# Performance work log

Measured on AMD Instinct MI355X. Metric: run time of the kernel, lower is better.

## Reference

```python
import jax, jax.numpy as jnp
import numpy as np

N = 100000   # nodes
E = 1600000  # directed edges (before self loops)
IN = 64
HID = 32     # per-head hidden channels
H = 4        # heads
OUT = 32     # final output channels
NEG_SLOPE = 0.2
LN_EPS = 1e-5


def setup_inputs() -> dict:
    key = jax.random.key(0)
    ks = jax.random.split(key, 24)
    def nrm(k, shape, s=0.1):
        return jax.random.normal(k, shape, jnp.float32) * s
    inp = {
        "x": jax.random.normal(ks[0], (N, IN), jnp.float32),
        "edge_index": jax.random.randint(ks[1], (2, E), 0, N, jnp.int32),
    }
    in_dims = [IN, H * HID, H * HID]
    j = 2
    for i, di in enumerate(in_dims):
        inp[f"W{i}"] = nrm(ks[j], (di, H * HID)); j += 1
        inp[f"as{i}"] = nrm(ks[j], (H, HID)); j += 1
        inp[f"ad{i}"] = nrm(ks[j], (H, HID)); j += 1
        inp[f"b{i}"] = jnp.zeros((H * HID,), jnp.float32)
        inp[f"g{i}"] = jnp.ones((H * HID,), jnp.float32)
        inp[f"be{i}"] = jnp.zeros((H * HID,), jnp.float32)
    inp["Wf"] = nrm(ks[j], (H * HID, OUT)); j += 1
    inp["asf"] = nrm(ks[j], (1, OUT)); j += 1
    inp["adf"] = nrm(ks[j], (1, OUT)); j += 1
    inp["bf"] = jnp.zeros((OUT,), jnp.float32)
    return inp


def gat_conv(x, src, dst, W, att_s, att_d, bias, heads, C, concat, n_nodes):
    # h: [N, H, C]
    h = (x @ W).reshape(n_nodes, heads, C)
    a_src = jnp.sum(h * att_s, axis=-1)  # [N, H]
    a_dst = jnp.sum(h * att_d, axis=-1)  # [N, H]
    e = jax.nn.leaky_relu(a_src[src] + a_dst[dst], NEG_SLOPE)  # [E', H]
    # segment softmax over incoming edges of each dst node
    m = jax.ops.segment_max(e, dst, num_segments=n_nodes)
    m = jnp.where(jnp.isfinite(m), m, 0.0)
    ex = jnp.exp(e - m[dst])
    denom = jax.ops.segment_sum(ex, dst, num_segments=n_nodes)
    alpha = ex / (denom[dst] + 1e-16)  # [E', H]
    msg = h[src] * alpha[..., None]    # [E', H, C]
    out = jax.ops.segment_sum(msg, dst, num_segments=n_nodes)  # [N, H, C]
    if concat:
        out = out.reshape(n_nodes, heads * C)
    else:
        out = out.mean(axis=1)
    return out + bias


def layer_norm(x, g, b):
    mu = x.mean(-1, keepdims=True)
    v = jnp.mean((x - mu) ** 2, axis=-1, keepdims=True)
    return g * (x - mu) / jnp.sqrt(v + LN_EPS) + b


def reference(x, edge_index,
              W0, as0, ad0, b0, g0, be0,
              W1, as1, ad1, b1, g1, be1,
              W2, as2, ad2, b2, g2, be2,
              Wf, asf, adf, bf):
    n_nodes = x.shape[0]
    loop = jnp.arange(n_nodes, dtype=edge_index.dtype)
    src = jnp.concatenate([edge_index[0], loop])  # add self loops (PyG default)
    dst = jnp.concatenate([edge_index[1], loop])
    blocks = [(W0, as0, ad0, b0, g0, be0),
              (W1, as1, ad1, b1, g1, be1),
              (W2, as2, ad2, b2, g2, be2)]
    for (W, a_s, a_d, b, g, be) in blocks:
        x = gat_conv(x, src, dst, W, a_s, a_d, b, H, HID, True, n_nodes)
        x = jax.nn.elu(layer_norm(x, g, be))
    return gat_conv(x, src, dst, Wf, asf, adf, bf, 1, OUT, False, n_nodes)
```

## Files before the change

### kernel.cpp

```cpp
#include <hip/hip_runtime.h>
#include <hip/hip_fp16.h>

constexpr int NN   = 100000;
constexpr int EE   = 1600000;
constexpr int ETOT = EE + NN;
constexpr float SLOPE = 0.2f;
constexpr int BSH = 10;
constexpr int NB  = (NN + (1 << BSH) - 1) >> BSH;
constexpr int CCH = 8192;
constexpr int DCAP  = 36;
constexpr int DCAPP = 37;

typedef __attribute__((ext_vector_type(8))) short short8;
typedef __attribute__((ext_vector_type(4))) float f32x4;

__device__ __forceinline__ unsigned short f2h(float f) {
    __half h = __float2half(f);
    return *(unsigned short*)&h;
}
__device__ __forceinline__ float h_lo(unsigned u) {
    unsigned short s = u & 0xffff;
    return __half2float(*(__half*)&s);
}
__device__ __forceinline__ float h_hi(unsigned u) {
    unsigned short s = u >> 16;
    return __half2float(*(__half*)&s);
}
__device__ __forceinline__ void wave_lds_fence() {
    __asm__ volatile("s_waitcnt lgkmcnt(0)" ::: "memory");
}
__device__ __forceinline__ void pk8(__half2* acc2, uint4 u, __half2 a2) {
    acc2[0] = __hfma2(*(__half2*)&u.x, a2, acc2[0]);
    acc2[1] = __hfma2(*(__half2*)&u.y, a2, acc2[1]);
    acc2[2] = __hfma2(*(__half2*)&u.z, a2, acc2[2]);
    acc2[3] = __hfma2(*(__half2*)&u.w, a2, acc2[3]);
}
__device__ __forceinline__ void fma8f(float* acc, uint4 u, float al) {
    acc[0] += h_lo(u.x) * al; acc[1] += h_hi(u.x) * al;
    acc[2] += h_lo(u.y) * al; acc[3] += h_hi(u.y) * al;
    acc[4] += h_lo(u.z) * al; acc[5] += h_hi(u.z) * al;
    acc[6] += h_lo(u.w) * al; acc[7] += h_hi(u.w) * al;
}

__global__ void k_cvt_x(const float* __restrict__ x, unsigned short* __restrict__ xb) {
    int i = blockIdx.x * blockDim.x + threadIdx.x;
    if (i >= NN * 64 / 8) return;
    const float4* xp = (const float4*)(x + (size_t)i * 8);
    float4 v0 = xp[0], v1 = xp[1];
    unsigned short o[8] = {f2h(v0.x), f2h(v0.y), f2h(v0.z), f2h(v0.w),
                           f2h(v1.x), f2h(v1.y), f2h(v1.z), f2h(v1.w)};
    *(uint4*)(xb + (size_t)i * 8) = *(uint4*)o;
}

__global__ void k_cvt_wt(const float* __restrict__ W, unsigned short* __restrict__ Wt,
                         int K, int N) {
    int i = blockIdx.x * blockDim.x + threadIdx.x;
    if (i >= K * N) return;
    int k = i / N, n = i % N;
    Wt[(size_t)n * K + k] = f2h(W[i]);
}

__global__ void k_zero(int* p, int n) {
    int i = blockIdx.x * blockDim.x + threadIdx.x;
    if (i < n) p[i] = 0;
}

__global__ __launch_bounds__(256) void k_bhist(const int* __restrict__ ei,
                                               int* __restrict__ gbh) {
    __shared__ int h[NB];
    int t = threadIdx.x;
    if (t < NB) h[t] = 0;
    __syncthreads();
    int i = blockIdx.x * 2048 + t;
#pragma unroll
    for (int k = 0; k < 8; k++, i += 256)
        if (i < EE) atomicAdd(&h[ei[EE + i] >> BSH], 1);
    __syncthreads();
    if (t < NB && h[t]) atomicAdd(&gbh[t], h[t]);
}

__global__ void k_bscan(const int* __restrict__ gbh, int* __restrict__ ebase,
                        int* __restrict__ gcur) {
    __shared__ int sd[128];
    int t = threadIdx.x;
    int v = (t < NB) ? gbh[t] : 0;
    sd[t] = v;
    __syncthreads();
    for (int off = 1; off < 128; off <<= 1) {
        int x = (t >= off) ? sd[t - off] : 0;
        __syncthreads();
        sd[t] += x;
        __syncthreads();
    }
    int ex = sd[t] - v;
    if (t < NB) { ebase[t] = ex; gcur[t] = ex; }
    if (t == NB) ebase[NB] = EE;
}

__global__ __launch_bounds__(256) void k_bscatter(const int* __restrict__ ei,
                                                  int* __restrict__ gcur,
                                                  int* __restrict__ pbuf) {
    __shared__ int h[NB], base[NB], cur[NB];
    int t = threadIdx.x;
    if (t < NB) { h[t] = 0; cur[t] = 0; }
    __syncthreads();
    int c0 = blockIdx.x * CCH;
    int cend = c0 + CCH < EE ? c0 + CCH : EE;
    for (int i = c0 + t; i < cend; i += 256)
        atomicAdd(&h[ei[EE + i] >> BSH], 1);
    __syncthreads();
    if (t < NB && h[t] > 0) base[t] = atomicAdd(&gcur[t], h[t]);
    __syncthreads();
    for (int i = c0 + t; i < cend; i += 256) {
        int s = ei[i], d = ei[EE + i];
        int b = d >> BSH;
        int c = atomicAdd(&cur[b], 1);
        pbuf[base[b] + c] = s | ((d & ((1 << BSH) - 1)) << 17);
    }
}

__global__ __launch_bounds__(256) void k_bcsr(const int* __restrict__ pbuf,
                                              const int* __restrict__ ebase,
                                              int* __restrict__ row_ptr,
                                              int* __restrict__ esrc) {
    constexpr int BNODES = 1 << BSH;
    __shared__ int hist[BNODES];
    __shared__ int cur[BNODES];
    __shared__ int sd[256];
    int b = blockIdx.x, t = threadIdx.x;
    int node0 = b << BSH;
    int e0 = ebase[b], e1 = ebase[b + 1];
    for (int i = t; i < BNODES; i += 256) { hist[i] = 0; cur[i] = 0; }
    __syncthreads();
    for (int i = e0 + t; i < e1; i += 256)
        atomicAdd(&hist[pbuf[i] >> 17], 1);
    __syncthreads();
    int s0 = hist[4 * t], s1 = hist[4 * t + 1], s2 = hist[4 * t + 2], s3 = hist[4 * t + 3];
    int ts = s0 + s1 + s2 + s3;
    sd[t] = ts;
    __syncthreads();
    for (int off = 1; off < 256; off <<= 1) {
        int x = (t >= off) ? sd[t - off] : 0;
        __syncthreads();
        sd[t] += x;
        __syncthreads();
    }
    int ex = sd[t] - ts;
    hist[4 * t] = ex;
    hist[4 * t + 1] = ex + s0;
    hist[4 * t + 2] = ex + s0 + s1;
    hist[4 * t + 3] = ex + s0 + s1 + s2;
    __syncthreads();
    int rbase = e0 + node0;
    for (int nl = t; nl < BNODES; nl += 256) {
        int n = node0 + nl;
        if (n < NN) {
            int rp = rbase + hist[nl] + nl;
            row_ptr[n] = rp;
            esrc[rp] = n;
        }
    }
    __syncthreads();
    for (int i = e0 + t; i < e1; i += 256) {
        int p = pbuf[i];
        int nl = p >> 17;
        int c = atomicAdd(&cur[nl], 1);
        esrc[rbase + hist[nl] + nl + 1 + c] = p & 0x1FFFF;
    }
}

template <int BN, int H>
__global__ __launch_bounds__(256) void k_mfma_att(
    const unsigned short* __restrict__ Ab, const unsigned short* __restrict__ Bt,
    const float* __restrict__ as_, const float* __restrict__ ad_,
    unsigned short* __restrict__ hb, float* __restrict__ a_s,
    float* __restrict__ a_d, int M, int K) {
    constexpr int NCT = BN / 16;
    constexpr int LDK = 72;
    __shared__ unsigned short As[128 * LDK];
    __shared__ unsigned short Bs[BN * LDK];
    int tid = threadIdx.x;
    int lane = tid & 63, w = tid >> 6;
    int q = lane >> 4, col = lane & 15;
    int rowBase = blockIdx.x * 128;

    f32x4 acc[2][NCT];
#pragma unroll
    for (int rt = 0; rt < 2; rt++)
#pragma unroll
        for (int ct = 0; ct < NCT; ct++) acc[rt][ct] = (f32x4){0.f, 0.f, 0.f, 0.f};

    int u = tid & 7;
    int r0 = tid >> 3;
    int nph = K >> 6;
    for (int ph = 0; ph < nph; ph++) {
        int kof = ph * 64 + u * 8;
#pragma unroll
        for (int rr = r0; rr < 128; rr += 32) {
            int gr = rowBase + rr;
            uint4 v = make_uint4(0, 0, 0, 0);
            if (gr < M) v = *(const uint4*)(Ab + (size_t)gr * K + kof);
            *(uint4*)(&As[rr * LDK + u * 8]) = v;
        }
#pragma unroll
        for (int br = r0; br < BN; br += 32) {
            uint4 v = *(const uint4*)(Bt + (size_t)br * K + kof);
            *(uint4*)(&Bs[br * LDK + u * 8]) = v;
        }
        __syncthreads();

        short8 af[2][2];
#pragma unroll
        for (int rt = 0; rt < 2; rt++)
#pragma unroll
            for (int kt = 0; kt < 2; kt++)
                af[rt][kt] = *(const short8*)(&As[(w * 32 + rt * 16 + col) * LDK + kt * 32 + q * 8]);
#pragma unroll
        for (int kt = 0; kt < 2; kt++)
#pragma unroll
            for (int ct = 0; ct < NCT; ct++) {
                short8 bf = *(const short8*)(&Bs[(ct * 16 + col) * LDK + kt * 32 + q * 8]);
#pragma unroll
                for (int rt = 0; rt < 2; rt++)
                    acc[rt][ct] = __builtin_amdgcn_mfma_f32_16x16x32_f16(
                        af[rt][kt], bf, acc[rt][ct], 0, 0, 0);
            }
        __syncthreads();
    }

    float swv[NCT], dwv[NCT];
#pragma unroll
    for (int ct = 0; ct < NCT; ct++) {
        int c = ct * 16 + col;
        swv[ct] = as_[c];
        dwv[ct] = ad_[c];
    }
#pragma unroll
    for (int rt = 0; rt < 2; rt++) {
#pragma unroll
        for (int r = 0; r < 4; r++) {
            int gr = rowBase + w * 32 + rt * 16 + q * 4 + r;
            if constexpr (H == 4) {
                float ps[4] = {0, 0, 0, 0}, pd[4] = {0, 0, 0, 0};
#pragma unroll
                for (int ct = 0; ct < NCT; ct++) {
                    float v = acc[rt][ct][r];
                    ps[ct >> 1] += v * swv[ct];
                    pd[ct >> 1] += v * dwv[ct];
                }
#pragma unroll
                for (int m = 1; m < 16; m <<= 1)
#pragma unroll
                    for (int h = 0; h < 4; h++) {
                        ps[h] += __shfl_xor(ps[h], m);
                        pd[h] += __shfl_xor(pd[h], m);
                    }
                if (gr < M) {
#pragma unroll
                    for (int ct = 0; ct < NCT; ct++)
                        hb[(size_t)gr * BN + ct * 16 + col] = f2h(acc[rt][ct][r]);
                    if (col == 0) {
                        *(float4*)(a_s + (size_t)gr * 4) = make_float4(ps[0], ps[1], ps[2], ps[3]);
                        *(float4*)(a_d + (size_t)gr * 4) = make_float4(pd[0], pd[1], pd[2], pd[3]);
                    }
                }
            } else {
                float ps = 0.f, pd = 0.f;
#pragma unroll
                for (int ct = 0; ct < NCT; ct++) {
                    float v = acc[rt][ct][r];
                    ps += v * swv[ct];
                    pd += v * dwv[ct];
                }
#pragma unroll
                for (int m = 1; m < 16; m <<= 1) {
                    ps += __shfl_xor(ps, m);
                    pd += __shfl_xor(pd, m);
                }
                if (gr < M) {
#pragma unroll
                    for (int ct = 0; ct < NCT; ct++)
                        hb[(size_t)gr * BN + ct * 16 + col] = f2h(acc[rt][ct][r]);
                    if (col == 0) { a_s[gr] = ps; a_d[gr] = pd; }
                }
            }
        }
    }
}

__global__ __launch_bounds__(256) void k_aggregate_ln(
    const unsigned short* __restrict__ hb, const float* __restrict__ a_src,
    const float* __restrict__ a_dst, const int* __restrict__ row_ptr,
    const int* __restrict__ esrc, const float* __restrict__ bias,
    const float* __restrict__ gamma, const float* __restrict__ beta,
    unsigned short* __restrict__ xb) {
    __shared__ uint2 slab_all[4][4 * 4 * DCAPP];
    int tid = threadIdx.x;
    int w = tid >> 6, lane = tid & 63;
    int g = lane >> 4, i = lane & 15;
    int myhead = i >> 2;
    uint2* slab = slab_all[w];
    int n0 = blockIdx.x * 16 + w * 4;
    int n = n0 + g;
    bool valid = n < NN;
    int start = 0, deg = 0;
    if (valid) {
        start = row_ptr[n];
        int end = (n == NN - 1) ? ETOT : row_ptr[n + 1];
        deg = end - start;
    }
    int wmax = deg;
#pragma unroll
    for (int m = 1; m < 64; m <<= 1) wmax = max(wmax, __shfl_xor(wmax, m));

    if (wmax <= DCAP) {
        float4 ad = make_float4(0.f, 0.f, 0.f, 0.f);
        if (valid) ad = ((const float4*)a_dst)[n];
        float d0 = 0.f, d1 = 0.f, d2 = 0.f, d3 = 0.f;
        uint2* nslab = slab + g * (4 * DCAPP);
        for (int k = i; k < deg; k += 16) {
            int s = esrc[start + k];
            float4 a = ((const float4*)a_src)[s];
            float e0 = a.x + ad.x; e0 = fmaxf(e0, SLOPE * e0); float x0 = __expf(e0);
            float e1 = a.y + ad.y; e1 = fmaxf(e1, SLOPE * e1); float x1 = __expf(e1);
            float e2 = a.z + ad.z; e2 = fmaxf(e2, SLOPE * e2); float x2 = __expf(e2);
            float e3 = a.w + ad.w; e3 = fmaxf(e3, SLOPE * e3); float x3 = __expf(e3);
            nslab[0 * DCAPP + k] = make_uint2((unsigned)s, __float_as_uint(x0));
            nslab[1 * DCAPP + k] = make_uint2((unsigned)s, __float_as_uint(x1));
            nslab[2 * DCAPP + k] = make_uint2((unsigned)s, __float_as_uint(x2));
            nslab[3 * DCAPP + k] = make_uint2((unsigned)s, __float_as_uint(x3));
            d0 += x0; d1 += x1; d2 += x2; d3 += x3;
        }
#pragma unroll
        for (int m = 1; m < 16; m <<= 1) {
            d0 += __shfl_xor(d0, m);
            d1 += __shfl_xor(d1, m);
            d2 += __shfl_xor(d2, m);
            d3 += __shfl_xor(d3, m);
        }
        float dh = myhead == 0 ? d0 : myhead == 1 ? d1 : myhead == 2 ? d2 : d3;
        float inv = 1.f / (dh + 1e-16f);
        wave_lds_fence();

        __half2 acc2[4];
#pragma unroll
        for (int k = 0; k < 4; k++) acc2[k] = __float2half2_rn(0.f);
        const uint2* myrow = nslab + myhead * DCAPP;
        const unsigned short* hbase = hb + i * 8;
        int j = 0;
        for (; j + 4 <= deg; j += 4) {
            uint2 p0 = myrow[j], p1 = myrow[j + 1], p2 = myrow[j + 2], p3 = myrow[j + 3];
            uint4 u0 = *(const uint4*)(hbase + (size_t)p0.x * 128);
            uint4 u1 = *(const uint4*)(hbase + (size_t)p1.x * 128);
            uint4 u2 = *(const uint4*)(hbase + (size_t)p2.x * 128);
            uint4 u3 = *(const uint4*)(hbase + (size_t)p3.x * 128);
            pk8(acc2, u0, __float2half2_rn(__uint_as_float(p0.y)));
            pk8(acc2, u1, __float2half2_rn(__uint_as_float(p1.y)));
            pk8(acc2, u2, __float2half2_rn(__uint_as_float(p2.y)));
            pk8(acc2, u3, __float2half2_rn(__uint_as_float(p3.y)));
        }
        for (; j < deg; j++) {
            uint2 p = myrow[j];
            uint4 uu = *(const uint4*)(hbase + (size_t)p.x * 128);
            pk8(acc2, uu, __float2half2_rn(__uint_as_float(p.y)));
        }
        float acc[8];
#pragma unroll
        for (int k = 0; k < 4; k++) {
            float2 f = __half22float2(acc2[k]);
            acc[2 * k] = f.x * inv;
            acc[2 * k + 1] = f.y * inv;
        }

        if (valid) {
            float y[8];
            float sum = 0.f;
            const float4* bp = (const float4*)(bias + i * 8);
            float4 b0 = bp[0], b1 = bp[1];
#pragma unroll
            for (int k = 0; k < 8; k++) {
                float b = k < 4 ? (&b0.x)[k] : (&b1.x)[k - 4];
                y[k] = acc[k] + b;
                sum += y[k];
            }
#pragma unroll
            for (int m = 1; m < 16; m <<= 1) sum += __shfl_xor(sum, m);
            float mu = sum * (1.f / 128.f);
            float ss = 0.f;
            float d[8];
#pragma unroll
            for (int k = 0; k < 8; k++) { d[k] = y[k] - mu; ss += d[k] * d[k]; }
#pragma unroll
            for (int m = 1; m < 16; m <<= 1) ss += __shfl_xor(ss, m);
            float is = rsqrtf(ss * (1.f / 128.f) + 1e-5f);
            const float4* gp = (const float4*)(gamma + i * 8);
            const float4* ep = (const float4*)(beta + i * 8);
            float4 g0 = gp[0], g1 = gp[1], e0 = ep[0], e1 = ep[1];
            unsigned short o16[8];
#pragma unroll
            for (int k = 0; k < 8; k++) {
                float gm = k < 4 ? (&g0.x)[k] : (&g1.x)[k - 4];
                float bt = k < 4 ? (&e0.x)[k] : (&e1.x)[k - 4];
                float z = gm * (d[k] * is) + bt;
                o16[k] = f2h(z > 0.f ? z : __expf(z) - 1.f);
            }
            *(uint4*)(xb + (size_t)n * 128 + i * 8) = *(uint4*)o16;
        }
    } else {
        for (int m4 = 0; m4 < 4; m4++) {
            int nm = n0 + m4;
            if (nm >= NN) continue;
            int startm = row_ptr[nm];
            int endm = (nm == NN - 1) ? ETOT : row_ptr[nm + 1];
            int degm = endm - startm;
            float4 ad = ((const float4*)a_dst)[nm];
            int gg = lane >> 4, c16 = lane & 15, hh = c16 >> 2;
            float acc[8];
#pragma unroll
            for (int k = 0; k < 8; k++) acc[k] = 0.f;
            if (degm <= 64) {
                int msrc = 0;
                float me0 = 0.f, me1 = 0.f, me2 = 0.f, me3 = 0.f;
                if (lane < degm) {
                    int s = esrc[startm + lane];
                    msrc = s;
                    float4 a = ((const float4*)a_src)[s];
                    float e0 = a.x + ad.x; e0 = fmaxf(e0, SLOPE * e0); me0 = __expf(e0);
                    float e1 = a.y + ad.y; e1 = fmaxf(e1, SLOPE * e1); me1 = __expf(e1);
                    float e2 = a.z + ad.z; e2 = fmaxf(e2, SLOPE * e2); me2 = __expf(e2);
                    float e3 = a.w + ad.w; e3 = fmaxf(e3, SLOPE * e3); me3 = __expf(e3);
                }
                float d0 = me0, d1 = me1, d2 = me2, d3 = me3;
#pragma unroll
                for (int m = 1; m < 64; m <<= 1) {
                    d0 += __shfl_xor(d0, m);
                    d1 += __shfl_xor(d1, m);
                    d2 += __shfl_xor(d2, m);
                    d3 += __shfl_xor(d3, m);
                }
                me0 *= 1.f / (d0 + 1e-16f);
                me1 *= 1.f / (d1 + 1e-16f);
                me2 *= 1.f / (d2 + 1e-16f);
                me3 *= 1.f / (d3 + 1e-16f);
                int iters = (degm + 3) >> 2;
                for (int it = 0; it < iters; it++) {
                    int j = gg + (it << 2);
                    int jj = j < degm ? j : 0;
                    int s = __shfl(msrc, jj);
                    float a0 = __shfl(me0, jj), a1 = __shfl(me1, jj);
                    float a2 = __shfl(me2, jj), a3 = __shfl(me3, jj);
                    if (j < degm) {
                        float al = hh == 0 ? a0 : hh == 1 ? a1 : hh == 2 ? a2 : a3;
                        uint4 uu = *(const uint4*)(hb + (size_t)s * 128 + c16 * 8);
                        fma8f(acc, uu, al);
                    }
                }
            } else {
                float d0 = 0.f, d1 = 0.f, d2 = 0.f, d3 = 0.f;
                for (int k = startm + lane; k < endm; k += 64) {
                    int s = esrc[k];
                    float4 a = ((const float4*)a_src)[s];
                    float e0 = a.x + ad.x; e0 = fmaxf(e0, SLOPE * e0); d0 += __expf(e0);
                    float e1 = a.y + ad.y; e1 = fmaxf(e1, SLOPE * e1); d1 += __expf(e1);
                    float e2 = a.z + ad.z; e2 = fmaxf(e2, SLOPE * e2); d2 += __expf(e2);
                    float e3 = a.w + ad.w; e3 = fmaxf(e3, SLOPE * e3); d3 += __expf(e3);
                }
#pragma unroll
                for (int m = 1; m < 64; m <<= 1) {
                    d0 += __shfl_xor(d0, m);
                    d1 += __shfl_xor(d1, m);
                    d2 += __shfl_xor(d2, m);
                    d3 += __shfl_xor(d3, m);
                }
                float invh = hh == 0 ? 1.f / (d0 + 1e-16f) : hh == 1 ? 1.f / (d1 + 1e-16f)
                           : hh == 2 ? 1.f / (d2 + 1e-16f) : 1.f / (d3 + 1e-16f);
                float adh = hh == 0 ? ad.x : hh == 1 ? ad.y : hh == 2 ? ad.z : ad.w;
                for (int j = gg; j < degm; j += 4) {
                    int s = esrc[startm + j];
                    float e = a_src[(size_t)s * 4 + hh] + adh;
                    e = fmaxf(e, SLOPE * e);
                    float al = __expf(e) * invh;
                    uint4 uu = *(const uint4*)(hb + (size_t)s * 128 + c16 * 8);
                    fma8f(acc, uu, al);
                }
            }
#pragma unroll
            for (int k = 0; k < 8; k++) {
                acc[k] += __shfl_xor(acc[k], 16);
                acc[k] += __shfl_xor(acc[k], 32);
            }
            if (lane < 16) {
                float y[8];
                float sum = 0.f;
                const float4* bp = (const float4*)(bias + lane * 8);
                float4 b0 = bp[0], b1 = bp[1];
#pragma unroll
                for (int k = 0; k < 8; k++) {
                    float b = k < 4 ? (&b0.x)[k] : (&b1.x)[k - 4];
                    y[k] = acc[k] + b;
                    sum += y[k];
                }
#pragma unroll
                for (int m = 1; m < 16; m <<= 1) sum += __shfl_xor(sum, m);
                float mu = sum * (1.f / 128.f);
                float ss = 0.f;
                float d[8];
#pragma unroll
                for (int k = 0; k < 8; k++) { d[k] = y[k] - mu; ss += d[k] * d[k]; }
#pragma unroll
                for (int m = 1; m < 16; m <<= 1) ss += __shfl_xor(ss, m);
                float is = rsqrtf(ss * (1.f / 128.f) + 1e-5f);
                const float4* gp = (const float4*)(gamma + lane * 8);
                const float4* ep = (const float4*)(beta + lane * 8);
                float4 g0 = gp[0], g1 = gp[1], e0 = ep[0], e1 = ep[1];
                unsigned short o16[8];
#pragma unroll
                for (int k = 0; k < 8; k++) {
                    float gm = k < 4 ? (&g0.x)[k] : (&g1.x)[k - 4];
                    float bt = k < 4 ? (&e0.x)[k] : (&e1.x)[k - 4];
                    float z = gm * (d[k] * is) + bt;
                    o16[k] = f2h(z > 0.f ? z : __expf(z) - 1.f);
                }
                *(uint4*)(xb + (size_t)nm * 128 + lane * 8) = *(uint4*)o16;
            }
        }
    }
}

__global__ __launch_bounds__(256) void k_agg_final(
    const unsigned short* __restrict__ hb, const float* __restrict__ a_src,
    const float* __restrict__ a_dst, const int* __restrict__ row_ptr,
    const int* __restrict__ esrc, const float* __restrict__ bf,
    float* __restrict__ out) {
    __shared__ uint2 slab_all[4][64];
    int lane = threadIdx.x & 63;
    int w = threadIdx.x >> 6;
    uint2* slab = slab_all[w];
    int n = blockIdx.x * 4 + w;
    if (n >= NN) return;
    int start = row_ptr[n];
    int end = (n == NN - 1) ? ETOT : row_ptr[n + 1];
    int deg = end - start;
    float adn = a_dst[n];

    int g = lane >> 3, c8 = lane & 7;
    float acc[4] = {0.f, 0.f, 0.f, 0.f};

    if (deg <= 64) {
        int msrc = 0;
        float me = 0.f;
        if (lane < deg) {
            int s = esrc[start + lane];
            msrc = s;
            float e = a_src[s] + adn;
            e = fmaxf(e, SLOPE * e);
            me = __expf(e);
        }
        float d = me;
#pragma unroll
        for (int m = 1; m < 64; m <<= 1) d += __shfl_xor(d, m);
        float inv = 1.f / (d + 1e-16f);
        if (lane < deg) slab[lane] = make_uint2((unsigned)msrc, __float_as_uint(me));
        wave_lds_fence();
        __half2 acc2[2] = {__float2half2_rn(0.f), __float2half2_rn(0.f)};
        const unsigned short* hbase = hb + c8 * 4;
        int j = g;
        for (; j + 8 < deg; j += 16) {
            uint2 p0 = slab[j], p1 = slab[j + 8];
            uint2 u0 = *(const uint2*)(hbase + (size_t)p0.x * 32);
            uint2 u1 = *(const uint2*)(hbase + (size_t)p1.x * 32);
            __half2 a0 = __float2half2_rn(__uint_as_float(p0.y));
            __half2 a1 = __float2half2_rn(__uint_as_float(p1.y));
            acc2[0] = __hfma2(*(__half2*)&u0.x, a0, acc2[0]);
            acc2[1] = __hfma2(*(__half2*)&u0.y, a0, acc2[1]);
            acc2[0] = __hfma2(*(__half2*)&u1.x, a1, acc2[0]);
            acc2[1] = __hfma2(*(__half2*)&u1.y, a1, acc2[1]);
        }
        if (j < deg) {
            uint2 p = slab[j];
            uint2 u = *(const uint2*)(hbase + (size_t)p.x * 32);
            __half2 a2 = __float2half2_rn(__uint_as_float(p.y));
            acc2[0] = __hfma2(*(__half2*)&u.x, a2, acc2[0]);
            acc2[1] = __hfma2(*(__half2*)&u.y, a2, acc2[1]);
        }
        float2 f0 = __half22float2(acc2[0]);
        float2 f1 = __half22float2(acc2[1]);
        acc[0] = f0.x * inv; acc[1] = f0.y * inv;
        acc[2] = f1.x * inv; acc[3] = f1.y * inv;
    } else {
        float d = 0.f;
        for (int k = start + lane; k < end; k += 64) {
            int s = esrc[k];
            float e = a_src[s] + adn;
            e = fmaxf(e, SLOPE * e);
            d += __expf(e);
        }
#pragma unroll
        for (int m = 1; m < 64; m <<= 1) d += __shfl_xor(d, m);
        float inv = 1.f / (d + 1e-16f);
        for (int j = g; j < deg; j += 8) {
            int s = esrc[start + j];
            float e = a_src[s] + adn;
            e = fmaxf(e, SLOPE * e);
            float al = __expf(e) * inv;
            uint2 u = *(const uint2*)(hb + (size_t)s * 32 + c8 * 4);
            acc[0] += h_lo(u.x) * al; acc[1] += h_hi(u.x) * al;
            acc[2] += h_lo(u.y) * al; acc[3] += h_hi(u.y) * al;
        }
    }
#pragma unroll
    for (int k = 0; k < 4; k++) {
        acc[k] += __shfl_xor(acc[k], 8);
        acc[k] += __shfl_xor(acc[k], 16);
        acc[k] += __shfl_xor(acc[k], 32);
    }
    if (lane < 8) {
        float4 b4 = ((const float4*)bf)[lane];
        float4 o = make_float4(acc[0] + b4.x, acc[1] + b4.y, acc[2] + b4.z,
                               acc[3] + b4.w);
        ((float4*)out)[(size_t)n * 8 + lane] = o;
    }
}

extern "C" void kernel_launch(void* const* d_in, const int* in_sizes, int n_in,
                              void* d_out, int out_size, void* d_ws,
                              size_t ws_size, hipStream_t stream) {
    const float* x  = (const float*)d_in[0];
    const int* ei   = (const int*)d_in[1];
    const float* W[3]  = {(const float*)d_in[2], (const float*)d_in[8],  (const float*)d_in[14]};
    const float* AS[3] = {(const float*)d_in[3], (const float*)d_in[9],  (const float*)d_in[15]};
    const float* AD[3] = {(const float*)d_in[4], (const float*)d_in[10], (const float*)d_in[16]};
    const float* Bb[3] = {(const float*)d_in[5], (const float*)d_in[11], (const float*)d_in[17]};
    const float* G[3]  = {(const float*)d_in[6], (const float*)d_in[12], (const float*)d_in[18]};
    const float* BE[3] = {(const float*)d_in[7], (const float*)d_in[13], (const float*)d_in[19]};
    const float* Wf  = (const float*)d_in[20];
    const float* asf = (const float*)d_in[21];
    const float* adf = (const float*)d_in[22];
    const float* bfp = (const float*)d_in[23];
    float* out = (float*)d_out;

    unsigned short* xb = (unsigned short*)d_ws;
    unsigned short* hb = xb + (size_t)NN * 128;
    float* a_s = (float*)(hb + (size_t)NN * 128);
    float* a_d = a_s + (size_t)NN * 4;
    int* row_ptr = (int*)(a_d + (size_t)NN * 4);
    int* esrc    = row_ptr + NN;
    int* gbh     = esrc + ETOT;
    int* ebase   = gbh + NB;
    int* gcur    = ebase + NB + 1;
    int* pbuf    = gcur + NB;
    unsigned short* Wt0 = (unsigned short*)(pbuf + EE);
    unsigned short* Wt1 = Wt0 + 128 * 64;
    unsigned short* Wt2 = Wt1 + 128 * 128;
    unsigned short* Wtf = Wt2 + 128 * 128;

    k_cvt_x<<<(NN * 64 / 8 + 255) / 256, 256, 0, stream>>>(x, xb);
    k_cvt_wt<<<(64 * 128 + 255) / 256, 256, 0, stream>>>(W[0], Wt0, 64, 128);
    k_cvt_wt<<<(128 * 128 + 255) / 256, 256, 0, stream>>>(W[1], Wt1, 128, 128);
    k_cvt_wt<<<(128 * 128 + 255) / 256, 256, 0, stream>>>(W[2], Wt2, 128, 128);
    k_cvt_wt<<<(128 * 32 + 255) / 256, 256, 0, stream>>>(Wf, Wtf, 128, 32);

    k_zero<<<1, 128, 0, stream>>>(gbh, NB);
    k_bhist<<<(EE + 2047) / 2048, 256, 0, stream>>>(ei, gbh);
    k_bscan<<<1, 128, 0, stream>>>(gbh, ebase, gcur);
    k_bscatter<<<(EE + CCH - 1) / CCH, 256, 0, stream>>>(ei, gcur, pbuf);
    k_bcsr<<<NB, 256, 0, stream>>>(pbuf, ebase, row_ptr, esrc);

    const unsigned short* Wts[3] = {Wt0, Wt1, Wt2};
    int K = 64;
    int gblk = (NN + 127) / 128;
    for (int l = 0; l < 3; l++) {
        k_mfma_att<128, 4><<<gblk, 256, 0, stream>>>(xb, Wts[l], AS[l], AD[l],
                                                     hb, a_s, a_d, NN, K);
        k_aggregate_ln<<<(NN + 15) / 16, 256, 0, stream>>>(hb, a_s, a_d, row_ptr,
                                                           esrc, Bb[l], G[l], BE[l], xb);
        K = 128;
    }
    k_mfma_att<32, 1><<<gblk, 256, 0, stream>>>(xb, Wtf, asf, adf, hb, a_s, a_d,
                                                NN, 128);
    k_agg_final<<<(NN + 3) / 4, 256, 0, stream>>>(hb, a_s, a_d, row_ptr, esrc,
                                                  bfp, out);
}
```

Baseline: 552.4 us.

## Fuse x conversion into first GEMM, merge weight casts, sort CSR neighbor lists

Removes the separate fp32-to-fp16 conversion pass over x by converting while loading A tiles in the first GEMM. The four weight-transpose launches become one. In addition, each node's source list in the CSR is insertion-sorted in global memory so later gathers in the aggregation kernels hit nearby rows. The sorting adds serial per-thread work in k_bcsr, with about 16 entries per node.

```diff
diff --git a/kernel.cpp b/kernel.cpp
--- a/kernel.cpp
+++ b/kernel.cpp
@@ -42,22 +42,18 @@
     acc[6] += h_lo(u.w) * al; acc[7] += h_hi(u.w) * al;
 }
 
-__global__ void k_cvt_x(const float* __restrict__ x, unsigned short* __restrict__ xb) {
+__global__ void k_cvt_w4(const float* __restrict__ W0, const float* __restrict__ W1,
+                         const float* __restrict__ W2, const float* __restrict__ Wf,
+                         unsigned short* __restrict__ Wt0, unsigned short* __restrict__ Wt1,
+                         unsigned short* __restrict__ Wt2, unsigned short* __restrict__ Wtf) {
     int i = blockIdx.x * blockDim.x + threadIdx.x;
-    if (i >= NN * 64 / 8) return;
-    const float4* xp = (const float4*)(x + (size_t)i * 8);
-    float4 v0 = xp[0], v1 = xp[1];
-    unsigned short o[8] = {f2h(v0.x), f2h(v0.y), f2h(v0.z), f2h(v0.w),
-                           f2h(v1.x), f2h(v1.y), f2h(v1.z), f2h(v1.w)};
-    *(uint4*)(xb + (size_t)i * 8) = *(uint4*)o;
-}
-
-__global__ void k_cvt_wt(const float* __restrict__ W, unsigned short* __restrict__ Wt,
-                         int K, int N) {
-    int i = blockIdx.x * blockDim.x + threadIdx.x;
-    if (i >= K * N) return;
-    int k = i / N, n = i % N;
-    Wt[(size_t)n * K + k] = f2h(W[i]);
+    if (i < 8192) { int k = i / 128, n = i % 128; Wt0[n * 64 + k] = f2h(W0[i]); return; }
+    i -= 8192;
+    if (i < 16384) { int k = i / 128, n = i % 128; Wt1[n * 128 + k] = f2h(W1[i]); return; }
+    i -= 16384;
+    if (i < 16384) { int k = i / 128, n = i % 128; Wt2[n * 128 + k] = f2h(W2[i]); return; }
+    i -= 16384;
+    if (i < 4096) { int k = i / 32, n = i % 32; Wtf[n * 128 + k] = f2h(Wf[i]); }
 }
 
 __global__ void k_zero(int* p, int n) {
@@ -167,11 +163,27 @@
         int c = atomicAdd(&cur[nl], 1);
         esrc[rbase + hist[nl] + nl + 1 + c] = p & 0x1FFFF;
     }
-}
-
-template <int BN, int H>
+    __syncthreads();
+    for (int nl = t; nl < BNODES; nl += 256) {
+        int n = node0 + nl;
+        if (n >= NN) continue;
+        int base2 = rbase + hist[nl] + nl + 1;
+        int cnt = cur[nl];
+        for (int a = 1; a < cnt; a++) {
+            int v = esrc[base2 + a];
+            int bb = a - 1;
+            while (bb >= 0 && esrc[base2 + bb] > v) {
+                esrc[base2 + bb + 1] = esrc[base2 + bb];
+                bb--;
+            }
+            esrc[base2 + bb + 1] = v;
+        }
+    }
+}
+
+template <int BN, int H, bool AF32>
 __global__ __launch_bounds__(256) void k_mfma_att(
-    const unsigned short* __restrict__ Ab, const unsigned short* __restrict__ Bt,
+    const void* __restrict__ Aptr, const unsigned short* __restrict__ Bt,
     const float* __restrict__ as_, const float* __restrict__ ad_,
     unsigned short* __restrict__ hb, float* __restrict__ a_s,
     float* __restrict__ a_d, int M, int K) {
@@ -198,9 +210,22 @@
 #pragma unroll
         for (int rr = r0; rr < 128; rr += 32) {
             int gr = rowBase + rr;
-            uint4 v = make_uint4(0, 0, 0, 0);
-            if (gr < M) v = *(const uint4*)(Ab + (size_t)gr * K + kof);
-            *(uint4*)(&As[rr * LDK + u * 8]) = v;
+            if constexpr (AF32) {
+                const float* A = (const float*)Aptr;
+                unsigned short o[8] = {0, 0, 0, 0, 0, 0, 0, 0};
+                if (gr < M) {
+                    const float4* ap = (const float4*)(A + (size_t)gr * K + kof);
+                    float4 v0 = ap[0], v1 = ap[1];
+                    o[0] = f2h(v0.x); o[1] = f2h(v0.y); o[2] = f2h(v0.z); o[3] = f2h(v0.w);
+                    o[4] = f2h(v1.x); o[5] = f2h(v1.y); o[6] = f2h(v1.z); o[7] = f2h(v1.w);
+                }
+                *(uint4*)(&As[rr * LDK + u * 8]) = *(uint4*)o;
+            } else {
+                const unsigned short* A = (const unsigned short*)Aptr;
+                uint4 v = make_uint4(0, 0, 0, 0);
+                if (gr < M) v = *(const uint4*)(A + (size_t)gr * K + kof);
+                *(uint4*)(&As[rr * LDK + u * 8]) = v;
+            }
         }
 #pragma unroll
         for (int br = r0; br < BN; br += 32) {
@@ -654,11 +679,8 @@
     unsigned short* Wt2 = Wt1 + 128 * 128;
     unsigned short* Wtf = Wt2 + 128 * 128;
 
-    k_cvt_x<<<(NN * 64 / 8 + 255) / 256, 256, 0, stream>>>(x, xb);
-    k_cvt_wt<<<(64 * 128 + 255) / 256, 256, 0, stream>>>(W[0], Wt0, 64, 128);
-    k_cvt_wt<<<(128 * 128 + 255) / 256, 256, 0, stream>>>(W[1], Wt1, 128, 128);
-    k_cvt_wt<<<(128 * 128 + 255) / 256, 256, 0, stream>>>(W[2], Wt2, 128, 128);
-    k_cvt_wt<<<(128 * 32 + 255) / 256, 256, 0, stream>>>(Wf, Wtf, 128, 32);
+    k_cvt_w4<<<(45056 + 255) / 256, 256, 0, stream>>>(W[0], W[1], W[2], Wf,
+                                                      Wt0, Wt1, Wt2, Wtf);
 
     k_zero<<<1, 128, 0, stream>>>(gbh, NB);
     k_bhist<<<(EE + 2047) / 2048, 256, 0, stream>>>(ei, gbh);
@@ -666,18 +688,20 @@
     k_bscatter<<<(EE + CCH - 1) / CCH, 256, 0, stream>>>(ei, gcur, pbuf);
     k_bcsr<<<NB, 256, 0, stream>>>(pbuf, ebase, row_ptr, esrc);
 
-    const unsigned short* Wts[3] = {Wt0, Wt1, Wt2};
-    int K = 64;
     int gblk = (NN + 127) / 128;
-    for (int l = 0; l < 3; l++) {
-        k_mfma_att<128, 4><<<gblk, 256, 0, stream>>>(xb, Wts[l], AS[l], AD[l],
-                                                     hb, a_s, a_d, NN, K);
+    k_mfma_att<128, 4, true><<<gblk, 256, 0, stream>>>(x, Wt0, AS[0], AD[0],
+                                                       hb, a_s, a_d, NN, 64);
+    k_aggregate_ln<<<(NN + 15) / 16, 256, 0, stream>>>(hb, a_s, a_d, row_ptr,
+                                                       esrc, Bb[0], G[0], BE[0], xb);
+    const unsigned short* Wts[2] = {Wt1, Wt2};
+    for (int l = 1; l < 3; l++) {
+        k_mfma_att<128, 4, false><<<gblk, 256, 0, stream>>>(xb, Wts[l - 1], AS[l], AD[l],
+                                                            hb, a_s, a_d, NN, 128);
         k_aggregate_ln<<<(NN + 15) / 16, 256, 0, stream>>>(hb, a_s, a_d, row_ptr,
                                                            esrc, Bb[l], G[l], BE[l], xb);
-        K = 128;
-    }
-    k_mfma_att<32, 1><<<gblk, 256, 0, stream>>>(xb, Wtf, asf, adf, hb, a_s, a_d,
-                                                NN, 128);
+    }
+    k_mfma_att<32, 1, false><<<gblk, 256, 0, stream>>>(xb, Wtf, asf, adf, hb, a_s, a_d,
+                                                       NN, 128);
     k_agg_final<<<(NN + 3) / 4, 256, 0, stream>>>(hb, a_s, a_d, row_ptr, esrc,
                                                   bfp, out);
 }
```

New measurement: 799.3 us. +44.7%, slower.
